# Performance work log

Measured on AMD Instinct MI355X. Metric: run time of the kernel, lower is better.

## Reference

```python
import jax, jax.numpy as jnp
import numpy as np

B = 16384
P = 16          # max_pos
D = 64          # per_digit_dim
C = 32          # carry_dim
N_OPS = 2
H = 256         # hidden
IN_DIM = 2 * D + N_OPS + C  # 162


def setup_inputs() -> dict:
    key = jax.random.key(0)
    ks = jax.random.split(key, 8)
    s1 = 1.0 / np.sqrt(IN_DIM)
    s2 = 1.0 / np.sqrt(H)
    return {
        "bias_a": jax.random.normal(ks[0], (B, P * D), dtype=jnp.float32),
        "bias_b": jax.random.normal(ks[1], (B, P * D), dtype=jnp.float32),
        "op": jax.random.uniform(ks[2], (B, N_OPS), dtype=jnp.float32),
        "W1": jax.random.normal(ks[3], (IN_DIM, H), dtype=jnp.float32) * s1,
        "b1": jnp.zeros((H,), dtype=jnp.float32),
        "W2": jax.random.normal(ks[4], (H, H), dtype=jnp.float32) * s2,
        "b2": jnp.zeros((H,), dtype=jnp.float32),
        "W3": jax.random.normal(ks[5], (H, D + C), dtype=jnp.float32) * s2,
        "b3": jnp.zeros((D + C,), dtype=jnp.float32),
    }


def reference(bias_a, bias_b, op, W1, b1, W2, b2, W3, b3):
    # [B, P*D] -> [P, B, D] for scanning over digit slots (low -> high)
    a = bias_a.reshape(B, P, D).transpose(1, 0, 2)
    b = bias_b.reshape(B, P, D).transpose(1, 0, 2)

    def step(carry, ab):
        a_i, b_i = ab
        x = jnp.concatenate([a_i, b_i, op, carry], axis=-1)  # [B, IN_DIM]
        h = jax.nn.relu(x @ W1 + b1)
        h = jax.nn.relu(h @ W2 + b2)
        y = h @ W3 + b3                                      # [B, D+C]
        return y[:, D:], y[:, :D]

    carry0 = jnp.zeros((B, C), dtype=bias_a.dtype)
    _, outs = jax.lax.scan(step, carry0, (a, b))             # outs: [P, B, D]
    return outs.transpose(1, 0, 2).reshape(B, P * D)
```

## Files before the change

### kernel.cpp

```cpp
#include <hip/hip_runtime.h>


typedef __attribute__((ext_vector_type(8))) short bf16x8;
typedef __attribute__((ext_vector_type(4))) float f32x4;
typedef __attribute__((ext_vector_type(2))) unsigned int u32x2;
typedef __attribute__((ext_vector_type(4))) unsigned int u32x4;

#define LDS_XAB 0
#define LDS_XC  16384
#define LDS_H1  24576
#define LDS_H2  57344
#define LDS_W3  90112
#define LDS_TOTAL 139264

__device__ inline unsigned short f32_to_bf16(float f) {
  unsigned int u = __builtin_bit_cast(unsigned int, f);
  u += 0x7FFFu + ((u >> 16) & 1u);
  return (unsigned short)(u >> 16);
}

__device__ inline unsigned int cvt_pk_bf16(float lo, float hi) {
  unsigned int r;
  asm("v_cvt_pk_bf16_f32 %0, %1, %2" : "=v"(r) : "v"(lo), "v"(hi));
  return r;
}

__global__ void pack_weights_kernel(const float* __restrict__ W1,
                                    const float* __restrict__ W2,
                                    const float* __restrict__ W3,
                                    unsigned short* __restrict__ wp) {
  int idx = blockIdx.x * 256 + threadIdx.x;
  if (idx >= 139264) return;
  int j, lane, frag, nt, kk, k, n;
  float v = 0.0f;
  if (idx < 49152) {
    int e = idx;
    j = e & 7; lane = (e >> 3) & 63; frag = e >> 9;
    nt = frag % 16; kk = frag / 16;
    k = kk * 32 + ((lane >> 4) << 3) + j;
    n = nt * 16 + (lane & 15);
    int ksrc;
    if (k < 128)      ksrc = k;
    else if (k < 160) ksrc = 130 + (k - 128);
    else if (k < 162) ksrc = 128 + (k - 160);
    else              ksrc = -1;
    v = (ksrc >= 0) ? W1[ksrc * 256 + n] : 0.0f;
  } else if (idx < 114688) {
    int e = idx - 49152;
    j = e & 7; lane = (e >> 3) & 63; frag = e >> 9;
    nt = frag % 16; kk = frag / 16;
    k = kk * 32 + ((lane >> 4) << 3) + j;
    n = nt * 16 + (lane & 15);
    v = W2[k * 256 + n];
  } else {
    int e = idx - 114688;
    j = e & 7; lane = (e >> 3) & 63; frag = e >> 9;
    nt = frag % 6; kk = frag / 6;
    k = kk * 32 + ((lane >> 4) << 3) + j;
    n = nt * 16 + (lane & 15);
    v = W3[k * 96 + n];
  }
  wp[idx] = f32_to_bf16(v);
}

__global__ __launch_bounds__(512, 2) void scan_kernel(
    const float* __restrict__ Ain, const float* __restrict__ Bin,
    const float* __restrict__ Op,
    const float* __restrict__ b1, const float* __restrict__ b2,
    const float* __restrict__ b3,
    const unsigned short* __restrict__ wp,
    float* __restrict__ out) {
  extern __shared__ char lds[];

  const int tid  = threadIdx.x;
  const int wave = tid >> 6, lane = tid & 63;
  const int lcol = lane & 15;
  const int q    = lane >> 4;
  const int row0 = blockIdx.x * 64;
  const int mw = wave >> 1, ngg = wave & 1;

  bf16x8 w1f[12], w2f[16];
  {
    const char* wb = (const char*)wp;
    #pragma unroll
    for (int kk = 0; kk < 6; ++kk)
      #pragma unroll
      for (int n = 0; n < 2; ++n)
        w1f[kk*2+n] = *(const bf16x8*)(wb + (size_t)(kk*16 + wave*2 + n)*1024 + lane*16);
    const char* wb2 = wb + 98304;
    #pragma unroll
    for (int kk = 0; kk < 8; ++kk)
      #pragma unroll
      for (int n = 0; n < 2; ++n)
        w2f[kk*2+n] = *(const bf16x8*)(wb2 + (size_t)(kk*16 + wave*2 + n)*1024 + lane*16);
  }
  f32x4 b1i[2], b2i[2], b3i[3];
  #pragma unroll
  for (int n = 0; n < 2; ++n)
    #pragma unroll
    for (int i = 0; i < 4; ++i) {
      b1i[n][i] = b1[(wave*2+n)*16 + q*4 + i];
      b2i[n][i] = b2[(wave*2+n)*16 + q*4 + i];
    }
  #pragma unroll
  for (int j = 0; j < 3; ++j)
    #pragma unroll
    for (int i = 0; i < 4; ++i)
      b3i[j][i] = b3[(ngg*3+j)*16 + q*4 + i];

  {
    const char* w3src = (const char*)wp + 229376;
    #pragma unroll
    for (int i = 0; i < 6; ++i)
      *(u32x4*)(lds + LDS_W3 + (size_t)(tid + i*512)*16) =
          *(const u32x4*)(w3src + (size_t)(tid + i*512)*16);
  }
  for (int i = tid; i < 4096; i += 512) {
    int r = i >> 6, kx = i & 63;
    unsigned short v = 0;
    if (kx == 32 || kx == 33) v = f32_to_bf16(Op[(size_t)(row0 + r)*2 + (kx - 32)]);
    int chunk = kx >> 3, within = (kx & 7) * 2;
    *(unsigned short*)(lds + LDS_XC + r*128 + ((chunk ^ (r & 7)) << 4) + within) = v;
  }

  const int part = tid & 7;
  const int srow = tid >> 3;
  const float* srcp = (part < 4 ? Ain : Bin) + (size_t)(row0 + srow)*1024 + (part & 3)*16;
  float4 pf[4];

  {
    #pragma unroll
    for (int jj = 0; jj < 4; ++jj) pf[jj] = *(const float4*)(srcp + jj*4);
    unsigned int u[8];
    #pragma unroll
    for (int jj = 0; jj < 4; ++jj) {
      u[jj*2]   = cvt_pk_bf16(pf[jj].x, pf[jj].y);
      u[jj*2+1] = cvt_pk_bf16(pf[jj].z, pf[jj].w);
    }
    u32x4 t0 = {u[0],u[1],u[2],u[3]}, t1 = {u[4],u[5],u[6],u[7]};
    *(u32x4*)(lds + LDS_XAB + srow*256 + (((part*2)   ^ (srow & 15)) << 4)) = t0;
    *(u32x4*)(lds + LDS_XAB + srow*256 + (((part*2+1) ^ (srow & 15)) << 4)) = t1;
    #pragma unroll
    for (int jj = 0; jj < 4; ++jj) pf[jj] = *(const float4*)(srcp + 64 + jj*4);
  }
  __syncthreads();

  #pragma unroll 1
  for (int p = 0; p < 16; ++p) {
    {
      f32x4 acc[2][4];
      #pragma unroll
      for (int n = 0; n < 2; ++n)
        #pragma unroll
        for (int m = 0; m < 4; ++m) acc[n][m] = b1i[n];
      #pragma unroll
      for (int m = 0; m < 4; ++m) {
        const int r = m*16 + lcol;
        bf16x8 xf[6];
        #pragma unroll
        for (int kk = 0; kk < 4; ++kk)
          xf[kk] = *(const bf16x8*)(lds + LDS_XAB + r*256 + (((4*kk + q) ^ lcol) << 4));
        #pragma unroll
        for (int kk = 0; kk < 2; ++kk)
          xf[4+kk] = *(const bf16x8*)(lds + LDS_XC + r*128 + (((4*kk + q) ^ (lcol & 7)) << 4));
        __builtin_amdgcn_s_setprio(1);
        #pragma unroll
        for (int kk = 0; kk < 6; ++kk) {
          acc[0][m] = __builtin_amdgcn_mfma_f32_16x16x32_bf16(w1f[kk*2+0], xf[kk], acc[0][m], 0,0,0);
          acc[1][m] = __builtin_amdgcn_mfma_f32_16x16x32_bf16(w1f[kk*2+1], xf[kk], acc[1][m], 0,0,0);
        }
        __builtin_amdgcn_s_setprio(0);
      }
      #pragma unroll
      for (int n = 0; n < 2; ++n) {
        const int nbyte = (wave*2+n)*32 + q*8;
        const int chunk = nbyte >> 4, within = nbyte & 15;
        #pragma unroll
        for (int m = 0; m < 4; ++m) {
          const int r = m*16 + lcol;
          float v0 = fmaxf(acc[n][m][0], 0.f);
          float v1 = fmaxf(acc[n][m][1], 0.f);
          float v2 = fmaxf(acc[n][m][2], 0.f);
          float v3 = fmaxf(acc[n][m][3], 0.f);
          u32x2 t; t.x = cvt_pk_bf16(v0, v1); t.y = cvt_pk_bf16(v2, v3);
          *(u32x2*)(lds + LDS_H1 + r*512 + ((chunk ^ lcol) << 4) + within) = t;
        }
      }
    }
    __syncthreads();

    if (p < 15) {
      unsigned int u[8];
      #pragma unroll
      for (int jj = 0; jj < 4; ++jj) {
        u[jj*2]   = cvt_pk_bf16(pf[jj].x, pf[jj].y);
        u[jj*2+1] = cvt_pk_bf16(pf[jj].z, pf[jj].w);
      }
      u32x4 t0 = {u[0],u[1],u[2],u[3]}, t1 = {u[4],u[5],u[6],u[7]};
      *(u32x4*)(lds + LDS_XAB + srow*256 + (((part*2)   ^ (srow & 15)) << 4)) = t0;
      *(u32x4*)(lds + LDS_XAB + srow*256 + (((part*2+1) ^ (srow & 15)) << 4)) = t1;
      if (p < 14) {
        const float* s2 = srcp + (p+2)*64;
        #pragma unroll
        for (int jj = 0; jj < 4; ++jj) pf[jj] = *(const float4*)(s2 + jj*4);
      }
    }

    {
      f32x4 acc[2][4];
      #pragma unroll
      for (int n = 0; n < 2; ++n)
        #pragma unroll
        for (int m = 0; m < 4; ++m) acc[n][m] = b2i[n];
      #pragma unroll
      for (int m = 0; m < 4; ++m) {
        const int r = m*16 + lcol;
        bf16x8 hf[8];
        #pragma unroll
        for (int kk = 0; kk < 8; ++kk)
          hf[kk] = *(const bf16x8*)(lds + LDS_H1 + r*512 + (((4*kk + q) ^ lcol) << 4));
        __builtin_amdgcn_s_setprio(1);
        #pragma unroll
        for (int kk = 0; kk < 8; ++kk) {
          acc[0][m] = __builtin_amdgcn_mfma_f32_16x16x32_bf16(w2f[kk*2+0], hf[kk], acc[0][m], 0,0,0);
          acc[1][m] = __builtin_amdgcn_mfma_f32_16x16x32_bf16(w2f[kk*2+1], hf[kk], acc[1][m], 0,0,0);
        }
        __builtin_amdgcn_s_setprio(0);
      }
      #pragma unroll
      for (int n = 0; n < 2; ++n) {
        const int nbyte = (wave*2+n)*32 + q*8;
        const int chunk = nbyte >> 4, within = nbyte & 15;
        #pragma unroll
        for (int m = 0; m < 4; ++m) {
          const int r = m*16 + lcol;
          float v0 = fmaxf(acc[n][m][0], 0.f);
          float v1 = fmaxf(acc[n][m][1], 0.f);
          float v2 = fmaxf(acc[n][m][2], 0.f);
          float v3 = fmaxf(acc[n][m][3], 0.f);
          u32x2 t; t.x = cvt_pk_bf16(v0, v1); t.y = cvt_pk_bf16(v2, v3);
          *(u32x2*)(lds + LDS_H2 + r*512 + ((chunk ^ lcol) << 4) + within) = t;
        }
      }
    }
    __syncthreads();

    {
      f32x4 acc3[3] = {b3i[0], b3i[1], b3i[2]};
      const int r = mw*16 + lcol;
      #pragma unroll
      for (int kk = 0; kk < 8; ++kk) {
        bf16x8 hf = *(const bf16x8*)(lds + LDS_H2 + r*512 + (((4*kk + q) ^ lcol) << 4));
        #pragma unroll
        for (int j = 0; j < 3; ++j) {
          bf16x8 wf = *(const bf16x8*)(lds + LDS_W3 + (size_t)(kk*6 + ngg*3 + j)*1024 + lane*16);
          acc3[j] = __builtin_amdgcn_mfma_f32_16x16x32_bf16(wf, hf, acc3[j], 0,0,0);
        }
      }
      #pragma unroll
      for (int j = 0; j < 3; ++j) {
        const int nt = ngg*3 + j;
        if (nt < 4) {
          float4 o;
          o.x = acc3[j][0]; o.y = acc3[j][1]; o.z = acc3[j][2]; o.w = acc3[j][3];
          *(float4*)&out[(size_t)(row0 + r)*1024 + p*64 + nt*16 + q*4] = o;
        } else {
          const int kbyte = (nt-4)*32 + q*8;
          const int chunk = kbyte >> 4, within = kbyte & 15;
          u32x2 t;
          t.x = cvt_pk_bf16(acc3[j][0], acc3[j][1]);
          t.y = cvt_pk_bf16(acc3[j][2], acc3[j][3]);
          *(u32x2*)(lds + LDS_XC + r*128 + ((chunk ^ (r & 7)) << 4) + within) = t;
        }
      }
    }
    __syncthreads();
  }
}

extern "C" void kernel_launch(void* const* d_in, const int* in_sizes, int n_in,
                              void* d_out, int out_size, void* d_ws, size_t ws_size,
                              hipStream_t stream) {
  const float* bias_a = (const float*)d_in[0];
  const float* bias_b = (const float*)d_in[1];
  const float* op     = (const float*)d_in[2];
  const float* W1     = (const float*)d_in[3];
  const float* b1     = (const float*)d_in[4];
  const float* W2     = (const float*)d_in[5];
  const float* b2     = (const float*)d_in[6];
  const float* W3     = (const float*)d_in[7];
  const float* b3     = (const float*)d_in[8];
  float* out = (float*)d_out;
  unsigned short* wp = (unsigned short*)d_ws;

  hipFuncSetAttribute((const void*)scan_kernel,
                      hipFuncAttributeMaxDynamicSharedMemorySize, LDS_TOTAL);

  pack_weights_kernel<<<544, 256, 0, stream>>>(W1, W2, W3, wp);
  scan_kernel<<<256, 512, LDS_TOTAL, stream>>>(bias_a, bias_b, op, b1, b2, b3, wp, out);
}
```

Baseline: 80.07 us.

## Read W3 from global memory instead of LDS and skew per-wave row order

Drops the W3 copy in LDS, cutting LDS use from about 136KB to 88KB per block, and reads the layer-3 weight fragments straight from global memory (L2/L1 cached) in the final matmul. The freed LDS could allow more blocks per CU. The order in which each wave walks its row tiles is also rotated per wave in layers 1 and 2, spreading LDS bank and port traffic across waves. In exchange, the layer-3 weight loads now carry global-memory latency on every scan step.

Result: slower. 255.8 us (+219.4%).

```diff
diff --git a/kernel.cpp b/kernel.cpp
--- a/kernel.cpp
+++ b/kernel.cpp
@@ -10,8 +10,7 @@
 #define LDS_XC  16384
 #define LDS_H1  24576
 #define LDS_H2  57344
-#define LDS_W3  90112
-#define LDS_TOTAL 139264
+#define LDS_TOTAL 90112
 
 __device__ inline unsigned short f32_to_bf16(float f) {
   unsigned int u = __builtin_bit_cast(unsigned int, f);
@@ -78,6 +77,7 @@
   const int q    = lane >> 4;
   const int row0 = blockIdx.x * 64;
   const int mw = wave >> 1, ngg = wave & 1;
+  const int skew2 = ((wave ^ (wave >> 2)) & 1) << 1;
 
   bf16x8 w1f[12], w2f[16];
   {
@@ -94,6 +94,8 @@
       for (int n = 0; n < 2; ++n)
         w2f[kk*2+n] = *(const bf16x8*)(wb2 + (size_t)(kk*16 + wave*2 + n)*1024 + lane*16);
   }
+  const char* w3g = (const char*)wp + 229376 + (size_t)(ngg*3)*1024 + (size_t)lane*16;
+
   f32x4 b1i[2], b2i[2], b3i[3];
   #pragma unroll
   for (int n = 0; n < 2; ++n)
@@ -108,13 +110,6 @@
     for (int i = 0; i < 4; ++i)
       b3i[j][i] = b3[(ngg*3+j)*16 + q*4 + i];
 
-  {
-    const char* w3src = (const char*)wp + 229376;
-    #pragma unroll
-    for (int i = 0; i < 6; ++i)
-      *(u32x4*)(lds + LDS_W3 + (size_t)(tid + i*512)*16) =
-          *(const u32x4*)(w3src + (size_t)(tid + i*512)*16);
-  }
   for (int i = tid; i < 4096; i += 512) {
     int r = i >> 6, kx = i & 63;
     unsigned short v = 0;
@@ -152,9 +147,10 @@
       #pragma unroll
       for (int n = 0; n < 2; ++n)
         #pragma unroll
-        for (int m = 0; m < 4; ++m) acc[n][m] = b1i[n];
-      #pragma unroll
-      for (int m = 0; m < 4; ++m) {
+        for (int mi = 0; mi < 4; ++mi) acc[n][mi] = b1i[n];
+      #pragma unroll
+      for (int mi = 0; mi < 4; ++mi) {
+        const int m = (mi + skew2) & 3;
         const int r = m*16 + lcol;
         bf16x8 xf[6];
         #pragma unroll
@@ -166,8 +162,8 @@
         __builtin_amdgcn_s_setprio(1);
         #pragma unroll
         for (int kk = 0; kk < 6; ++kk) {
-          acc[0][m] = __builtin_amdgcn_mfma_f32_16x16x32_bf16(w1f[kk*2+0], xf[kk], acc[0][m], 0,0,0);
-          acc[1][m] = __builtin_amdgcn_mfma_f32_16x16x32_bf16(w1f[kk*2+1], xf[kk], acc[1][m], 0,0,0);
+          acc[0][mi] = __builtin_amdgcn_mfma_f32_16x16x32_bf16(w1f[kk*2+0], xf[kk], acc[0][mi], 0,0,0);
+          acc[1][mi] = __builtin_amdgcn_mfma_f32_16x16x32_bf16(w1f[kk*2+1], xf[kk], acc[1][mi], 0,0,0);
         }
         __builtin_amdgcn_s_setprio(0);
       }
@@ -176,12 +172,12 @@
         const int nbyte = (wave*2+n)*32 + q*8;
         const int chunk = nbyte >> 4, within = nbyte & 15;
         #pragma unroll
-        for (int m = 0; m < 4; ++m) {
-          const int r = m*16 + lcol;
-          float v0 = fmaxf(acc[n][m][0], 0.f);
-          float v1 = fmaxf(acc[n][m][1], 0.f);
-          float v2 = fmaxf(acc[n][m][2], 0.f);
-          float v3 = fmaxf(acc[n][m][3], 0.f);
+        for (int mi = 0; mi < 4; ++mi) {
+          const int r = ((mi + skew2) & 3)*16 + lcol;
+          float v0 = fmaxf(acc[n][mi][0], 0.f);
+          float v1 = fmaxf(acc[n][mi][1], 0.f);
+          float v2 = fmaxf(acc[n][mi][2], 0.f);
+          float v3 = fmaxf(acc[n][mi][3], 0.f);
           u32x2 t; t.x = cvt_pk_bf16(v0, v1); t.y = cvt_pk_bf16(v2, v3);
           *(u32x2*)(lds + LDS_H1 + r*512 + ((chunk ^ lcol) << 4) + within) = t;
         }
@@ -211,9 +207,10 @@
       #pragma unroll
       for (int n = 0; n < 2; ++n)
         #pragma unroll
-        for (int m = 0; m < 4; ++m) acc[n][m] = b2i[n];
-      #pragma unroll
-      for (int m = 0; m < 4; ++m) {
+        for (int mi = 0; mi < 4; ++mi) acc[n][mi] = b2i[n];
+      #pragma unroll
+      for (int mi = 0; mi < 4; ++mi) {
+        const int m = (mi + skew2) & 3;
         const int r = m*16 + lcol;
         bf16x8 hf[8];
         #pragma unroll
@@ -222,8 +219,8 @@
         __builtin_amdgcn_s_setprio(1);
         #pragma unroll
         for (int kk = 0; kk < 8; ++kk) {
-          acc[0][m] = __builtin_amdgcn_mfma_f32_16x16x32_bf16(w2f[kk*2+0], hf[kk], acc[0][m], 0,0,0);
-          acc[1][m] = __builtin_amdgcn_mfma_f32_16x16x32_bf16(w2f[kk*2+1], hf[kk], acc[1][m], 0,0,0);
+          acc[0][mi] = __builtin_amdgcn_mfma_f32_16x16x32_bf16(w2f[kk*2+0], hf[kk], acc[0][mi], 0,0,0);
+          acc[1][mi] = __builtin_amdgcn_mfma_f32_16x16x32_bf16(w2f[kk*2+1], hf[kk], acc[1][mi], 0,0,0);
         }
         __builtin_amdgcn_s_setprio(0);
       }
@@ -232,12 +229,12 @@
         const int nbyte = (wave*2+n)*32 + q*8;
         const int chunk = nbyte >> 4, within = nbyte & 15;
         #pragma unroll
-        for (int m = 0; m < 4; ++m) {
-          const int r = m*16 + lcol;
-          float v0 = fmaxf(acc[n][m][0], 0.f);
-          float v1 = fmaxf(acc[n][m][1], 0.f);
-          float v2 = fmaxf(acc[n][m][2], 0.f);
-          float v3 = fmaxf(acc[n][m][3], 0.f);
+        for (int mi = 0; mi < 4; ++mi) {
+          const int r = ((mi + skew2) & 3)*16 + lcol;
+          float v0 = fmaxf(acc[n][mi][0], 0.f);
+          float v1 = fmaxf(acc[n][mi][1], 0.f);
+          float v2 = fmaxf(acc[n][mi][2], 0.f);
+          float v3 = fmaxf(acc[n][mi][3], 0.f);
           u32x2 t; t.x = cvt_pk_bf16(v0, v1); t.y = cvt_pk_bf16(v2, v3);
           *(u32x2*)(lds + LDS_H2 + r*512 + ((chunk ^ lcol) << 4) + within) = t;
         }
@@ -253,7 +250,7 @@
         bf16x8 hf = *(const bf16x8*)(lds + LDS_H2 + r*512 + (((4*kk + q) ^ lcol) << 4));
         #pragma unroll
         for (int j = 0; j < 3; ++j) {
-          bf16x8 wf = *(const bf16x8*)(lds + LDS_W3 + (size_t)(kk*6 + ngg*3 + j)*1024 + lane*16);
+          bf16x8 wf = *(const bf16x8*)(w3g + (size_t)(kk*6 + j)*1024);
           acc3[j] = __builtin_amdgcn_mfma_f32_16x16x32_bf16(wf, hf, acc3[j], 0,0,0);
         }
       }
```

## Specialize waves: six compute layer 3 from registers, two load next inputs

Applied to the files above, without the earlier changes.

W3 fragments move from LDS into registers, and layer 3 is split across six waves, each computing two row tiles by two column tiles. The remaining two waves load and convert the next digit's A/B inputs during that phase, replacing the register prefetch that every thread did between layers 1 and 2. Biases move from registers into LDS, and total LDS shrinks by about 46 KB. The changes aim to free LDS and remove the prefetch from the critical path. The cost is extra register pressure from w3f, and the input loads are no longer issued ahead of time, so their latency may be exposed.

Result: slower. 163.4 us (+104.0%).

```diff
diff --git a/kernel.cpp b/kernel.cpp
--- a/kernel.cpp
+++ b/kernel.cpp
@@ -10,8 +10,10 @@
 #define LDS_XC  16384
 #define LDS_H1  24576
 #define LDS_H2  57344
-#define LDS_W3  90112
-#define LDS_TOTAL 139264
+#define LDS_B1  90112
+#define LDS_B2  91136
+#define LDS_B3  92160
+#define LDS_TOTAL 92672
 
 __device__ inline unsigned short f32_to_bf16(float f) {
   unsigned int u = __builtin_bit_cast(unsigned int, f);
@@ -77,9 +79,10 @@
   const int lcol = lane & 15;
   const int q    = lane >> 4;
   const int row0 = blockIdx.x * 64;
-  const int mw = wave >> 1, ngg = wave & 1;
-
-  bf16x8 w1f[12], w2f[16];
+  const int n3 = wave % 3;
+  const int mh = wave / 3;
+
+  bf16x8 w1f[12], w2f[16], w3f[16];
   {
     const char* wb = (const char*)wp;
     #pragma unroll
@@ -93,28 +96,18 @@
       #pragma unroll
       for (int n = 0; n < 2; ++n)
         w2f[kk*2+n] = *(const bf16x8*)(wb2 + (size_t)(kk*16 + wave*2 + n)*1024 + lane*16);
-  }
-  f32x4 b1i[2], b2i[2], b3i[3];
-  #pragma unroll
-  for (int n = 0; n < 2; ++n)
-    #pragma unroll
-    for (int i = 0; i < 4; ++i) {
-      b1i[n][i] = b1[(wave*2+n)*16 + q*4 + i];
-      b2i[n][i] = b2[(wave*2+n)*16 + q*4 + i];
-    }
-  #pragma unroll
-  for (int j = 0; j < 3; ++j)
-    #pragma unroll
-    for (int i = 0; i < 4; ++i)
-      b3i[j][i] = b3[(ngg*3+j)*16 + q*4 + i];
-
-  {
-    const char* w3src = (const char*)wp + 229376;
-    #pragma unroll
-    for (int i = 0; i < 6; ++i)
-      *(u32x4*)(lds + LDS_W3 + (size_t)(tid + i*512)*16) =
-          *(const u32x4*)(w3src + (size_t)(tid + i*512)*16);
-  }
+    const char* wb3 = wb + 229376;
+    #pragma unroll
+    for (int kk = 0; kk < 8; ++kk)
+      #pragma unroll
+      for (int jn = 0; jn < 2; ++jn)
+        w3f[kk*2+jn] = *(const bf16x8*)(wb3 + (size_t)(kk*6 + n3*2 + jn)*1024 + lane*16);
+  }
+
+  if (tid < 256) ((float*)(lds + LDS_B1))[tid] = b1[tid];
+  else           ((float*)(lds + LDS_B2))[tid - 256] = b2[tid - 256];
+  if (tid < 96)  ((float*)(lds + LDS_B3))[tid] = b3[tid];
+
   for (int i = tid; i < 4096; i += 512) {
     int r = i >> 6, kx = i & 63;
     unsigned short v = 0;
@@ -123,25 +116,22 @@
     *(unsigned short*)(lds + LDS_XC + r*128 + ((chunk ^ (r & 7)) << 4) + within) = v;
   }
 
-  const int part = tid & 7;
-  const int srow = tid >> 3;
-  const float* srcp = (part < 4 ? Ain : Bin) + (size_t)(row0 + srow)*1024 + (part & 3)*16;
-  float4 pf[4];
-
   {
-    #pragma unroll
-    for (int jj = 0; jj < 4; ++jj) pf[jj] = *(const float4*)(srcp + jj*4);
+    const int part = tid & 7;
+    const int srow = tid >> 3;
+    const float* srcp = (part < 4 ? Ain : Bin) + (size_t)(row0 + srow)*1024 + (part & 3)*16;
+    float4 pv[4];
+    #pragma unroll
+    for (int jj = 0; jj < 4; ++jj) pv[jj] = *(const float4*)(srcp + jj*4);
     unsigned int u[8];
     #pragma unroll
     for (int jj = 0; jj < 4; ++jj) {
-      u[jj*2]   = cvt_pk_bf16(pf[jj].x, pf[jj].y);
-      u[jj*2+1] = cvt_pk_bf16(pf[jj].z, pf[jj].w);
+      u[jj*2]   = cvt_pk_bf16(pv[jj].x, pv[jj].y);
+      u[jj*2+1] = cvt_pk_bf16(pv[jj].z, pv[jj].w);
     }
     u32x4 t0 = {u[0],u[1],u[2],u[3]}, t1 = {u[4],u[5],u[6],u[7]};
     *(u32x4*)(lds + LDS_XAB + srow*256 + (((part*2)   ^ (srow & 15)) << 4)) = t0;
     *(u32x4*)(lds + LDS_XAB + srow*256 + (((part*2+1) ^ (srow & 15)) << 4)) = t1;
-    #pragma unroll
-    for (int jj = 0; jj < 4; ++jj) pf[jj] = *(const float4*)(srcp + 64 + jj*4);
   }
   __syncthreads();
 
@@ -149,10 +139,12 @@
   for (int p = 0; p < 16; ++p) {
     {
       f32x4 acc[2][4];
-      #pragma unroll
-      for (int n = 0; n < 2; ++n)
-        #pragma unroll
-        for (int m = 0; m < 4; ++m) acc[n][m] = b1i[n];
+      {
+        f32x4 bA = *(const f32x4*)(lds + LDS_B1 + (((wave*2+0)*16 + q*4) << 2));
+        f32x4 bB = *(const f32x4*)(lds + LDS_B1 + (((wave*2+1)*16 + q*4) << 2));
+        #pragma unroll
+        for (int mi = 0; mi < 4; ++mi) { acc[0][mi] = bA; acc[1][mi] = bB; }
+      }
       #pragma unroll
       for (int m = 0; m < 4; ++m) {
         const int r = m*16 + lcol;
@@ -189,29 +181,14 @@
     }
     __syncthreads();
 
-    if (p < 15) {
-      unsigned int u[8];
-      #pragma unroll
-      for (int jj = 0; jj < 4; ++jj) {
-        u[jj*2]   = cvt_pk_bf16(pf[jj].x, pf[jj].y);
-        u[jj*2+1] = cvt_pk_bf16(pf[jj].z, pf[jj].w);
-      }
-      u32x4 t0 = {u[0],u[1],u[2],u[3]}, t1 = {u[4],u[5],u[6],u[7]};
-      *(u32x4*)(lds + LDS_XAB + srow*256 + (((part*2)   ^ (srow & 15)) << 4)) = t0;
-      *(u32x4*)(lds + LDS_XAB + srow*256 + (((part*2+1) ^ (srow & 15)) << 4)) = t1;
-      if (p < 14) {
-        const float* s2 = srcp + (p+2)*64;
-        #pragma unroll
-        for (int jj = 0; jj < 4; ++jj) pf[jj] = *(const float4*)(s2 + jj*4);
-      }
-    }
-
     {
       f32x4 acc[2][4];
-      #pragma unroll
-      for (int n = 0; n < 2; ++n)
-        #pragma unroll
-        for (int m = 0; m < 4; ++m) acc[n][m] = b2i[n];
+      {
+        f32x4 bA = *(const f32x4*)(lds + LDS_B2 + (((wave*2+0)*16 + q*4) << 2));
+        f32x4 bB = *(const f32x4*)(lds + LDS_B2 + (((wave*2+1)*16 + q*4) << 2));
+        #pragma unroll
+        for (int mi = 0; mi < 4; ++mi) { acc[0][mi] = bA; acc[1][mi] = bB; }
+      }
       #pragma unroll
       for (int m = 0; m < 4; ++m) {
         const int r = m*16 + lcol;
@@ -245,33 +222,64 @@
     }
     __syncthreads();
 
-    {
-      f32x4 acc3[3] = {b3i[0], b3i[1], b3i[2]};
-      const int r = mw*16 + lcol;
-      #pragma unroll
-      for (int kk = 0; kk < 8; ++kk) {
-        bf16x8 hf = *(const bf16x8*)(lds + LDS_H2 + r*512 + (((4*kk + q) ^ lcol) << 4));
-        #pragma unroll
-        for (int j = 0; j < 3; ++j) {
-          bf16x8 wf = *(const bf16x8*)(lds + LDS_W3 + (size_t)(kk*6 + ngg*3 + j)*1024 + lane*16);
-          acc3[j] = __builtin_amdgcn_mfma_f32_16x16x32_bf16(wf, hf, acc3[j], 0,0,0);
-        }
-      }
-      #pragma unroll
-      for (int j = 0; j < 3; ++j) {
-        const int nt = ngg*3 + j;
-        if (nt < 4) {
-          float4 o;
-          o.x = acc3[j][0]; o.y = acc3[j][1]; o.z = acc3[j][2]; o.w = acc3[j][3];
-          *(float4*)&out[(size_t)(row0 + r)*1024 + p*64 + nt*16 + q*4] = o;
-        } else {
-          const int kbyte = (nt-4)*32 + q*8;
-          const int chunk = kbyte >> 4, within = kbyte & 15;
-          u32x2 t;
-          t.x = cvt_pk_bf16(acc3[j][0], acc3[j][1]);
-          t.y = cvt_pk_bf16(acc3[j][2], acc3[j][3]);
-          *(u32x2*)(lds + LDS_XC + r*128 + ((chunk ^ (r & 7)) << 4) + within) = t;
-        }
+    if (wave < 6) {
+      f32x4 acc3[2][2];
+      {
+        f32x4 c0 = *(const f32x4*)(lds + LDS_B3 + (((n3*2+0)*16 + q*4) << 2));
+        f32x4 c1 = *(const f32x4*)(lds + LDS_B3 + (((n3*2+1)*16 + q*4) << 2));
+        acc3[0][0] = c0; acc3[0][1] = c1; acc3[1][0] = c0; acc3[1][1] = c1;
+      }
+      #pragma unroll
+      for (int mi = 0; mi < 2; ++mi) {
+        const int r = (mh*2 + mi)*16 + lcol;
+        bf16x8 hf[8];
+        #pragma unroll
+        for (int kk = 0; kk < 8; ++kk)
+          hf[kk] = *(const bf16x8*)(lds + LDS_H2 + r*512 + (((4*kk + q) ^ lcol) << 4));
+        __builtin_amdgcn_s_setprio(1);
+        #pragma unroll
+        for (int kk = 0; kk < 8; ++kk) {
+          acc3[mi][0] = __builtin_amdgcn_mfma_f32_16x16x32_bf16(w3f[kk*2+0], hf[kk], acc3[mi][0], 0,0,0);
+          acc3[mi][1] = __builtin_amdgcn_mfma_f32_16x16x32_bf16(w3f[kk*2+1], hf[kk], acc3[mi][1], 0,0,0);
+        }
+        __builtin_amdgcn_s_setprio(0);
+      }
+      #pragma unroll
+      for (int jn = 0; jn < 2; ++jn) {
+        const int nt = n3*2 + jn;
+        #pragma unroll
+        for (int mi = 0; mi < 2; ++mi) {
+          const int r = (mh*2 + mi)*16 + lcol;
+          if (nt < 4) {
+            float4 o;
+            o.x = acc3[mi][jn][0]; o.y = acc3[mi][jn][1];
+            o.z = acc3[mi][jn][2]; o.w = acc3[mi][jn][3];
+            *(float4*)&out[(size_t)(row0 + r)*1024 + p*64 + nt*16 + q*4] = o;
+          } else {
+            const int kbyte = (nt-4)*32 + q*8;
+            const int chunk = kbyte >> 4, within = kbyte & 15;
+            u32x2 t;
+            t.x = cvt_pk_bf16(acc3[mi][jn][0], acc3[mi][jn][1]);
+            t.y = cvt_pk_bf16(acc3[mi][jn][2], acc3[mi][jn][3]);
+            *(u32x2*)(lds + LDS_XC + r*128 + ((chunk ^ (r & 7)) << 4) + within) = t;
+          }
+        }
+      }
+    } else if (p < 15) {
+      const int th = tid - 384;
+      const int sr = th & 63, half = th >> 6;
+      const float* sp = (half ? Bin : Ain) + (size_t)(row0 + sr)*1024 + (p+1)*64;
+      float4 v[16];
+      #pragma unroll
+      for (int j = 0; j < 16; ++j) v[j] = *(const float4*)(sp + j*4);
+      #pragma unroll
+      for (int j2 = 0; j2 < 8; ++j2) {
+        u32x4 t;
+        t.x = cvt_pk_bf16(v[2*j2].x,   v[2*j2].y);
+        t.y = cvt_pk_bf16(v[2*j2].z,   v[2*j2].w);
+        t.z = cvt_pk_bf16(v[2*j2+1].x, v[2*j2+1].y);
+        t.w = cvt_pk_bf16(v[2*j2+1].z, v[2*j2+1].w);
+        *(u32x4*)(lds + LDS_XAB + sr*256 + (((half*8 + j2) ^ (sr & 15)) << 4)) = t;
       }
     }
     __syncthreads();
```

## Keep W3 in registers with split-K layer-3 reduction through LDS

Applied to the files above, without the earlier changes.

Layer-3 weights move from LDS into per-wave registers. Layer 3 is repartitioned so wave pairs split the K dimension, and the partial sums are reduced through the H1 LDS region behind an extra barrier. Biases move from registers to LDS to free VGPRs, and the layer-2 fragment loads are split into two K halves to lower register pressure. This cuts per-step LDS weight reads and LDS footprint, at the cost of an added sync and reduction traffic each step.

New measurement: 118.4 us. 47.8% more time.

```diff
diff --git a/kernel.cpp b/kernel.cpp
--- a/kernel.cpp
+++ b/kernel.cpp
@@ -10,8 +10,10 @@
 #define LDS_XC  16384
 #define LDS_H1  24576
 #define LDS_H2  57344
-#define LDS_W3  90112
-#define LDS_TOTAL 139264
+#define LDS_B1  90112
+#define LDS_B2  91136
+#define LDS_B3  92160
+#define LDS_TOTAL 92672
 
 __device__ inline unsigned short f32_to_bf16(float f) {
   unsigned int u = __builtin_bit_cast(unsigned int, f);
@@ -77,9 +79,11 @@
   const int lcol = lane & 15;
   const int q    = lane >> 4;
   const int row0 = blockIdx.x * 64;
-  const int mw = wave >> 1, ngg = wave & 1;
-
-  bf16x8 w1f[12], w2f[16];
+  const int kh   = wave & 1;
+  const int sub3 = wave >> 1;
+  const int mh3  = sub3 >> 1, np3 = sub3 & 1;
+
+  bf16x8 w1f[12], w2f[16], w3f[12];
   {
     const char* wb = (const char*)wp;
     #pragma unroll
@@ -93,28 +97,18 @@
       #pragma unroll
       for (int n = 0; n < 2; ++n)
         w2f[kk*2+n] = *(const bf16x8*)(wb2 + (size_t)(kk*16 + wave*2 + n)*1024 + lane*16);
-  }
-  f32x4 b1i[2], b2i[2], b3i[3];
-  #pragma unroll
-  for (int n = 0; n < 2; ++n)
-    #pragma unroll
-    for (int i = 0; i < 4; ++i) {
-      b1i[n][i] = b1[(wave*2+n)*16 + q*4 + i];
-      b2i[n][i] = b2[(wave*2+n)*16 + q*4 + i];
-    }
-  #pragma unroll
-  for (int j = 0; j < 3; ++j)
-    #pragma unroll
-    for (int i = 0; i < 4; ++i)
-      b3i[j][i] = b3[(ngg*3+j)*16 + q*4 + i];
-
-  {
-    const char* w3src = (const char*)wp + 229376;
-    #pragma unroll
-    for (int i = 0; i < 6; ++i)
-      *(u32x4*)(lds + LDS_W3 + (size_t)(tid + i*512)*16) =
-          *(const u32x4*)(w3src + (size_t)(tid + i*512)*16);
-  }
+    const char* wb3 = wb + 229376;
+    #pragma unroll
+    for (int kk = 0; kk < 4; ++kk)
+      #pragma unroll
+      for (int j = 0; j < 3; ++j)
+        w3f[kk*3+j] = *(const bf16x8*)(wb3 + (size_t)((kh*4+kk)*6 + np3*3 + j)*1024 + lane*16);
+  }
+
+  if (tid < 256) ((float*)(lds + LDS_B1))[tid] = b1[tid];
+  else           ((float*)(lds + LDS_B2))[tid - 256] = b2[tid - 256];
+  if (tid < 96)  ((float*)(lds + LDS_B3))[tid] = b3[tid];
+
   for (int i = tid; i < 4096; i += 512) {
     int r = i >> 6, kx = i & 63;
     unsigned short v = 0;
@@ -145,14 +139,18 @@
   }
   __syncthreads();
 
+  const f32x4 zero4 = {0.f, 0.f, 0.f, 0.f};
+
   #pragma unroll 1
   for (int p = 0; p < 16; ++p) {
     {
       f32x4 acc[2][4];
-      #pragma unroll
-      for (int n = 0; n < 2; ++n)
-        #pragma unroll
-        for (int m = 0; m < 4; ++m) acc[n][m] = b1i[n];
+      {
+        f32x4 bA = *(const f32x4*)(lds + LDS_B1 + (((wave*2+0)*16 + q*4) << 2));
+        f32x4 bB = *(const f32x4*)(lds + LDS_B1 + (((wave*2+1)*16 + q*4) << 2));
+        #pragma unroll
+        for (int mi = 0; mi < 4; ++mi) { acc[0][mi] = bA; acc[1][mi] = bB; }
+      }
       #pragma unroll
       for (int m = 0; m < 4; ++m) {
         const int r = m*16 + lcol;
@@ -208,24 +206,29 @@
 
     {
       f32x4 acc[2][4];
-      #pragma unroll
-      for (int n = 0; n < 2; ++n)
-        #pragma unroll
-        for (int m = 0; m < 4; ++m) acc[n][m] = b2i[n];
+      {
+        f32x4 bA = *(const f32x4*)(lds + LDS_B2 + (((wave*2+0)*16 + q*4) << 2));
+        f32x4 bB = *(const f32x4*)(lds + LDS_B2 + (((wave*2+1)*16 + q*4) << 2));
+        #pragma unroll
+        for (int mi = 0; mi < 4; ++mi) { acc[0][mi] = bA; acc[1][mi] = bB; }
+      }
       #pragma unroll
       for (int m = 0; m < 4; ++m) {
         const int r = m*16 + lcol;
-        bf16x8 hf[8];
-        #pragma unroll
-        for (int kk = 0; kk < 8; ++kk)
-          hf[kk] = *(const bf16x8*)(lds + LDS_H1 + r*512 + (((4*kk + q) ^ lcol) << 4));
-        __builtin_amdgcn_s_setprio(1);
-        #pragma unroll
-        for (int kk = 0; kk < 8; ++kk) {
-          acc[0][m] = __builtin_amdgcn_mfma_f32_16x16x32_bf16(w2f[kk*2+0], hf[kk], acc[0][m], 0,0,0);
-          acc[1][m] = __builtin_amdgcn_mfma_f32_16x16x32_bf16(w2f[kk*2+1], hf[kk], acc[1][m], 0,0,0);
-        }
-        __builtin_amdgcn_s_setprio(0);
+        #pragma unroll
+        for (int kb = 0; kb < 2; ++kb) {
+          bf16x8 hf[4];
+          #pragma unroll
+          for (int kk = 0; kk < 4; ++kk)
+            hf[kk] = *(const bf16x8*)(lds + LDS_H1 + r*512 + (((4*(kb*4+kk) + q) ^ lcol) << 4));
+          __builtin_amdgcn_s_setprio(1);
+          #pragma unroll
+          for (int kk = 0; kk < 4; ++kk) {
+            acc[0][m] = __builtin_amdgcn_mfma_f32_16x16x32_bf16(w2f[(kb*4+kk)*2+0], hf[kk], acc[0][m], 0,0,0);
+            acc[1][m] = __builtin_amdgcn_mfma_f32_16x16x32_bf16(w2f[(kb*4+kk)*2+1], hf[kk], acc[1][m], 0,0,0);
+          }
+          __builtin_amdgcn_s_setprio(0);
+        }
       }
       #pragma unroll
       for (int n = 0; n < 2; ++n) {
@@ -246,31 +249,57 @@
     __syncthreads();
 
     {
-      f32x4 acc3[3] = {b3i[0], b3i[1], b3i[2]};
-      const int r = mw*16 + lcol;
-      #pragma unroll
-      for (int kk = 0; kk < 8; ++kk) {
-        bf16x8 hf = *(const bf16x8*)(lds + LDS_H2 + r*512 + (((4*kk + q) ^ lcol) << 4));
+      f32x4 acc3[2][3];
+      #pragma unroll
+      for (int mi = 0; mi < 2; ++mi)
+        #pragma unroll
+        for (int j = 0; j < 3; ++j) acc3[mi][j] = zero4;
+      #pragma unroll
+      for (int mi = 0; mi < 2; ++mi) {
+        const int r = (mh3*2 + mi)*16 + lcol;
+        bf16x8 hf[4];
+        #pragma unroll
+        for (int kk = 0; kk < 4; ++kk)
+          hf[kk] = *(const bf16x8*)(lds + LDS_H2 + r*512 + (((4*(kh*4+kk) + q) ^ lcol) << 4));
+        __builtin_amdgcn_s_setprio(1);
+        #pragma unroll
+        for (int kk = 0; kk < 4; ++kk)
+          #pragma unroll
+          for (int j = 0; j < 3; ++j)
+            acc3[mi][j] = __builtin_amdgcn_mfma_f32_16x16x32_bf16(w3f[kk*3+j], hf[kk], acc3[mi][j], 0,0,0);
+        __builtin_amdgcn_s_setprio(0);
+      }
+      if (kh) {
+        #pragma unroll
+        for (int mi = 0; mi < 2; ++mi)
+          #pragma unroll
+          for (int j = 0; j < 3; ++j)
+            *(f32x4*)(lds + LDS_H1 + (((sub3*6 + mi*3 + j) << 10) + lane*16)) = acc3[mi][j];
+      }
+      __syncthreads();
+      if (!kh) {
         #pragma unroll
         for (int j = 0; j < 3; ++j) {
-          bf16x8 wf = *(const bf16x8*)(lds + LDS_W3 + (size_t)(kk*6 + ngg*3 + j)*1024 + lane*16);
-          acc3[j] = __builtin_amdgcn_mfma_f32_16x16x32_bf16(wf, hf, acc3[j], 0,0,0);
-        }
-      }
-      #pragma unroll
-      for (int j = 0; j < 3; ++j) {
-        const int nt = ngg*3 + j;
-        if (nt < 4) {
-          float4 o;
-          o.x = acc3[j][0]; o.y = acc3[j][1]; o.z = acc3[j][2]; o.w = acc3[j][3];
-          *(float4*)&out[(size_t)(row0 + r)*1024 + p*64 + nt*16 + q*4] = o;
-        } else {
-          const int kbyte = (nt-4)*32 + q*8;
-          const int chunk = kbyte >> 4, within = kbyte & 15;
-          u32x2 t;
-          t.x = cvt_pk_bf16(acc3[j][0], acc3[j][1]);
-          t.y = cvt_pk_bf16(acc3[j][2], acc3[j][3]);
-          *(u32x2*)(lds + LDS_XC + r*128 + ((chunk ^ (r & 7)) << 4) + within) = t;
+          const int nt = np3*3 + j;
+          f32x4 bj = *(const f32x4*)(lds + LDS_B3 + ((nt*16 + q*4) << 2));
+          #pragma unroll
+          for (int mi = 0; mi < 2; ++mi) {
+            f32x4 part = *(const f32x4*)(lds + LDS_H1 + (((sub3*6 + mi*3 + j) << 10) + lane*16));
+            f32x4 v = acc3[mi][j] + part + bj;
+            const int r = (mh3*2 + mi)*16 + lcol;
+            if (nt < 4) {
+              float4 o;
+              o.x = v[0]; o.y = v[1]; o.z = v[2]; o.w = v[3];
+              *(float4*)&out[(size_t)(row0 + r)*1024 + p*64 + nt*16 + q*4] = o;
+            } else {
+              const int kbyte = (nt-4)*32 + q*8;
+              const int chunk = kbyte >> 4, within = kbyte & 15;
+              u32x2 t;
+              t.x = cvt_pk_bf16(v[0], v[1]);
+              t.y = cvt_pk_bf16(v[2], v[3]);
+              *(u32x2*)(lds + LDS_XC + r*128 + ((chunk ^ (r & 7)) << 4) + within) = t;
+            }
+          }
         }
       }
     }
```
